# Kernel tuning notes

Measured on AMD Instinct MI355X. Metric: run time of the kernel, lower is better.

Reference implementation:

```python
import jax, jax.numpy as jnp
import numpy as np

B = 131072   # batch
K = 3        # kernel size (= stride)
NP = 9       # num patches (9x9 image, 3x3 kernel, stride 3)
NU = 81      # num logic units/kernels
NOPS = 16    # real-valued binary logic ops


def setup_inputs() -> dict:
    key = jax.random.key(0)
    k1, k2, k3, k4 = jax.random.split(key, 4)
    x = jax.random.uniform(k1, (B, 1, 9, 9), dtype=jnp.float32)          # soft-binary image
    sel_a_logits = jax.random.normal(k2, (NU, K * K), dtype=jnp.float32)  # input-A selector per unit
    sel_b_logits = jax.random.normal(k3, (NU, K * K), dtype=jnp.float32)  # input-B selector per unit
    op_logits = jax.random.normal(k4, (NU, NOPS), dtype=jnp.float32)      # logic-op mixture per unit
    return {"x": x, "sel_a_logits": sel_a_logits, "sel_b_logits": sel_b_logits, "op_logits": op_logits}


def _soft_logic_mix(a, b, w):
    # a, b: [B, NU] soft-binary operands; w: [NU, 16] op mixture weights (broadcast over batch).
    # The 16 real-valued binary logic gates (Petersen et al. differentiable logic networks).
    ab = a * b
    return (w[:, 1] * ab
            + w[:, 2] * (a - ab)
            + w[:, 3] * a
            + w[:, 4] * (b - ab)
            + w[:, 5] * b
            + w[:, 6] * (a + b - 2.0 * ab)      # xor
            + w[:, 7] * (a + b - ab)            # or
            + w[:, 8] * (1.0 - (a + b - ab))    # nor
            + w[:, 9] * (1.0 - (a + b - 2.0 * ab))  # xnor
            + w[:, 10] * (1.0 - b)
            + w[:, 11] * (1.0 - b + ab)
            + w[:, 12] * (1.0 - a)
            + w[:, 13] * (1.0 - a + ab)
            + w[:, 14] * (1.0 - ab)             # nand
            + w[:, 15])                          # op 0 contributes 0


def reference(x, sel_a_logits, sel_b_logits, op_logits):
    b_sz = x.shape[0]
    img = x[:, 0]  # [B, 9, 9]
    # unfold(2,K,S).unfold(3,K,S) with S == K == 3 -> non-overlapping 3x3 patches, row-major patch order
    patches = img.reshape(b_sz, NP // K, K, NP // K, K)
    patches = patches.transpose(0, 1, 3, 2, 4).reshape(b_sz, NP, K * K)  # [B, 9, 9]
    # unit u uses patch u // kernels_per_pos (kernels_per_pos = 81 // 9 = 9)
    unit2patch = jnp.arange(NU) // (NU // NP)
    inp = patches[:, unit2patch]  # [B, 81, 9]
    a = jnp.einsum('bui,ui->bu', inp, jax.nn.softmax(sel_a_logits, axis=-1))  # [B, 81]
    b = jnp.einsum('bui,ui->bu', inp, jax.nn.softmax(sel_b_logits, axis=-1))  # [B, 81]
    w = jax.nn.softmax(op_logits, axis=-1)  # [81, 16]
    return _soft_logic_mix(a, b, w)  # [B, 81]
```

## Files before the change

kernel.cpp:

```cpp
#include <hip/hip_runtime.h>
#include <math.h>


#define NB      131072
#define NUNITS  81
#define BPB     64
#define THREADS 256
#define NBLK    (NB / BPB)
#define REC     24
#define CHUNKS  1296

__global__ __launch_bounds__(256)
void logic_prep_kernel(const float* __restrict__ sa_logits,
                       const float* __restrict__ sb_logits,
                       const float* __restrict__ op_logits,
                       float* __restrict__ tab)
{
    const int tid = threadIdx.x;
    if (tid < 81) {
        const int u = tid;
        float v[9], m = -1e30f;
        #pragma unroll
        for (int i = 0; i < 9; ++i) { v[i] = sa_logits[u * 9 + i]; m = fmaxf(m, v[i]); }
        float s = 0.f;
        #pragma unroll
        for (int i = 0; i < 9; ++i) { v[i] = expf(v[i] - m); s += v[i]; }
        const float r = 1.f / s;
        #pragma unroll
        for (int i = 0; i < 9; ++i) tab[u * REC + i] = v[i] * r;
    } else if (tid < 162) {
        const int u = tid - 81;
        float v[9], m = -1e30f;
        #pragma unroll
        for (int i = 0; i < 9; ++i) { v[i] = sb_logits[u * 9 + i]; m = fmaxf(m, v[i]); }
        float s = 0.f;
        #pragma unroll
        for (int i = 0; i < 9; ++i) { v[i] = expf(v[i] - m); s += v[i]; }
        const float r = 1.f / s;
        #pragma unroll
        for (int i = 0; i < 9; ++i) tab[u * REC + 9 + i] = v[i] * r;
    } else if (tid < 243) {
        const int u = tid - 162;
        float v[16], m = -1e30f;
        #pragma unroll
        for (int i = 0; i < 16; ++i) { v[i] = op_logits[u * 16 + i]; m = fmaxf(m, v[i]); }
        float s = 0.f;
        #pragma unroll
        for (int i = 0; i < 16; ++i) { v[i] = expf(v[i] - m); s += v[i]; }
        const float r = 1.f / s;
        #pragma unroll
        for (int i = 0; i < 16; ++i) v[i] *= r;
        const float cab = v[1] - v[2] - v[4] - 2.f*v[6] - v[7] + v[8] + 2.f*v[9]
                        + v[11] + v[13] - v[14];
        const float ca  = v[2] + v[3] + v[6] + v[7] - v[8] - v[9] - v[12] - v[13];
        const float cb  = v[4] + v[5] + v[6] + v[7] - v[8] - v[9] - v[10] - v[11];
        const float c0  = v[8] + v[9] + v[10] + v[11] + v[12] + v[13] + v[14] + v[15];
        tab[u * REC + 18] = cab;
        tab[u * REC + 19] = ca;
        tab[u * REC + 20] = cb;
        tab[u * REC + 21] = c0;
    }
}

__global__ __launch_bounds__(THREADS)
void logic_main_kernel(const float* __restrict__ x,
                       const float* __restrict__ tab,
                       float* __restrict__ out)
{
    __shared__ float s_tile[BPB * 81];

    const int tid  = threadIdx.x;
    const int lane = tid & 63;
    const int wavei = __builtin_amdgcn_readfirstlane(tid >> 6);
    const size_t b0 = (size_t)blockIdx.x * BPB;

    {
        const float4* gsrc = (const float4*)(x + b0 * 81);
        float4* s4 = (float4*)s_tile;
        #pragma unroll
        for (int k = 0; k < 6; ++k) {
            int j = tid + k * THREADS;
            if (j < CHUNKS) s4[j] = gsrc[j];
        }
    }
    __syncthreads();

    if (wavei < 3) {
        float* my = s_tile + lane * 81 + wavei * 27;

        float in[27];
        #pragma unroll
        for (int j = 0; j < 27; ++j) in[j] = my[j];

        const float* __restrict__ wt = tab + wavei * 27 * REC;

        #pragma unroll
        for (int j = 0; j < 27; ++j) {
            const int q = j / 9;
            const float* __restrict__ wr = wt + j * REC;
            float a = 0.f, b = 0.f;
            #pragma unroll
            for (int i = 0; i < 9; ++i) {
                const float xi = in[q * 3 + (i / 3) * 9 + (i % 3)];
                a = fmaf(xi, wr[i],     a);
                b = fmaf(xi, wr[9 + i], b);
            }
            const float ab = a * b;
            my[j] = fmaf(wr[18], ab, fmaf(wr[19], a, fmaf(wr[20], b, wr[21])));
        }
    }

    __syncthreads();

    {
        const float4* s4 = (const float4*)s_tile;
        float4* gdst = (float4*)(out + b0 * 81);
        #pragma unroll
        for (int k = 0; k < 6; ++k) {
            int j = tid + k * THREADS;
            if (j < CHUNKS) gdst[j] = s4[j];
        }
    }
}

extern "C" void kernel_launch(void* const* d_in, const int* in_sizes, int n_in,
                              void* d_out, int out_size, void* d_ws, size_t ws_size,
                              hipStream_t stream)
{
    const float* x  = (const float*)d_in[0];
    const float* sa = (const float*)d_in[1];
    const float* sb = (const float*)d_in[2];
    const float* op = (const float*)d_in[3];
    float* tab = (float*)d_ws;
    float* outp = (float*)d_out;

    logic_prep_kernel<<<1, 256, 0, stream>>>(sa, sb, op, tab);
    logic_main_kernel<<<NBLK, THREADS, 0, stream>>>(x, tab, outp);
}
```

Baseline: 32.80 us.

## Use one thread per batch row with direct global loads into registers

The main kernel now uses 64-thread blocks in which each thread computes all 81 units for one batch row. Each thread reads its 81 inputs straight from global memory into registers, so the shared-memory staging of the input tile and the first barrier go away. Previously only 3 of 4 waves computed. The output is still staged through shared memory for coalesced float4 stores. The per-thread global loads use an 81-float stride across lanes, which coalesces poorly, and the large register footprint may lower occupancy.

```diff
diff --git a/kernel.cpp b/kernel.cpp
--- a/kernel.cpp
+++ b/kernel.cpp
@@ -4,11 +4,10 @@
 
 #define NB      131072
 #define NUNITS  81
-#define BPB     64
-#define THREADS 256
-#define NBLK    (NB / BPB)
+#define THREADS 64
+#define NBLK    (NB / THREADS)
 #define REC     24
-#define CHUNKS  1296
+#define CHUNKS  (THREADS * 81 / 4)
 
 __global__ __launch_bounds__(256)
 void logic_prep_kernel(const float* __restrict__ sa_logits,
@@ -62,62 +61,47 @@
     }
 }
 
-__global__ __launch_bounds__(THREADS)
+__global__ __launch_bounds__(THREADS, 2)
 void logic_main_kernel(const float* __restrict__ x,
                        const float* __restrict__ tab,
                        float* __restrict__ out)
 {
-    __shared__ float s_tile[BPB * 81];
+    __shared__ float s_out[THREADS * 81];
 
-    const int tid  = threadIdx.x;
-    const int lane = tid & 63;
-    const int wavei = __builtin_amdgcn_readfirstlane(tid >> 6);
-    const size_t b0 = (size_t)blockIdx.x * BPB;
+    const int lane  = threadIdx.x;
+    const size_t b  = (size_t)blockIdx.x * THREADS + lane;
 
+    float in[81];
     {
-        const float4* gsrc = (const float4*)(x + b0 * 81);
-        float4* s4 = (float4*)s_tile;
+        const float* __restrict__ src = x + b * 81;
         #pragma unroll
-        for (int k = 0; k < 6; ++k) {
-            int j = tid + k * THREADS;
-            if (j < CHUNKS) s4[j] = gsrc[j];
+        for (int j = 0; j < 81; ++j) in[j] = src[j];
+    }
+
+    float* my = s_out + lane * 81;
+    #pragma unroll
+    for (int u = 0; u < NUNITS; ++u) {
+        const int p    = u / 9;
+        const int base = (p / 3) * 27 + (p % 3) * 3;
+        const float* __restrict__ wr = tab + u * REC;
+        float a = 0.f, bb = 0.f;
+        #pragma unroll
+        for (int i = 0; i < 9; ++i) {
+            const float xi = in[base + (i / 3) * 9 + (i % 3)];
+            a  = fmaf(xi, wr[i],     a);
+            bb = fmaf(xi, wr[9 + i], bb);
         }
-    }
-    __syncthreads();
-
-    if (wavei < 3) {
-        float* my = s_tile + lane * 81 + wavei * 27;
-
-        float in[27];
-        #pragma unroll
-        for (int j = 0; j < 27; ++j) in[j] = my[j];
-
-        const float* __restrict__ wt = tab + wavei * 27 * REC;
-
-        #pragma unroll
-        for (int j = 0; j < 27; ++j) {
-            const int q = j / 9;
-            const float* __restrict__ wr = wt + j * REC;
-            float a = 0.f, b = 0.f;
-            #pragma unroll
-            for (int i = 0; i < 9; ++i) {
-                const float xi = in[q * 3 + (i / 3) * 9 + (i % 3)];
-                a = fmaf(xi, wr[i],     a);
-                b = fmaf(xi, wr[9 + i], b);
-            }
-            const float ab = a * b;
-            my[j] = fmaf(wr[18], ab, fmaf(wr[19], a, fmaf(wr[20], b, wr[21])));
-        }
+        my[u] = fmaf(wr[18], a * bb, fmaf(wr[19], a, fmaf(wr[20], bb, wr[21])));
     }
 
     __syncthreads();
 
     {
-        const float4* s4 = (const float4*)s_tile;
-        float4* gdst = (float4*)(out + b0 * 81);
+        const float4* s4 = (const float4*)s_out;
+        float4* gdst = (float4*)(out + (size_t)blockIdx.x * THREADS * 81);
         #pragma unroll
-        for (int k = 0; k < 6; ++k) {
-            int j = tid + k * THREADS;
+        for (int k = 0; k < 21; ++k) {
+            const int j = k * THREADS + lane;
             if (j < CHUNKS) gdst[j] = s4[j];
         }
     }
@@ -131,7 +115,7 @@
     const float* sa = (const float*)d_in[1];
     const float* sb = (const float*)d_in[2];
     const float* op = (const float*)d_in[3];
-    float* tab = (float*)d_ws;
+    float* tab  = (float*)d_ws;
     float* outp = (float*)d_out;
 
     logic_prep_kernel<<<1, 256, 0, stream>>>(sa, sb, op, tab);
```

Result: slower. 43.11 us (+31.4%).
